# Kernel tuning notes

Measured on AMD Instinct MI355X. Metric: run time of the kernel, lower is better.

Reference implementation:

```python
import jax, jax.numpy as jnp
import numpy as np
import math

N_NODES = 50000
N_EDGES = 800000
DIM = 128
NUM_HEADS = 8
CUTOFF = 5.0


def setup_inputs() -> dict:
    key = jax.random.key(0)
    ks = jax.random.split(key, 12)
    s = 1.0 / math.sqrt(DIM)
    inp = {
        "x": jax.random.normal(ks[0], (N_NODES, DIM), dtype=jnp.float32),
        "edge_index": jax.random.randint(ks[1], (2, N_EDGES), 0, N_NODES, dtype=jnp.int32),
        "edge_attr": jax.random.normal(ks[2], (N_EDGES, DIM), dtype=jnp.float32),
        "edge_len": jax.random.uniform(ks[3], (N_EDGES,), dtype=jnp.float32) * CUTOFF,
        "W_Q": jax.random.normal(ks[4], (DIM, DIM), dtype=jnp.float32) * s,
        "b_Q": jnp.zeros((DIM,), dtype=jnp.float32),
        "W_K": jax.random.normal(ks[5], (DIM, DIM), dtype=jnp.float32) * s,
        "b_K": jnp.zeros((DIM,), dtype=jnp.float32),
        "W_V": jax.random.normal(ks[6], (DIM, DIM), dtype=jnp.float32) * s,
        "b_V": jnp.zeros((DIM,), dtype=jnp.float32),
        "W_O": jax.random.normal(ks[7], (DIM, DIM), dtype=jnp.float32) * s,
        "b_O": jnp.zeros((DIM,), dtype=jnp.float32),
    }
    return inp


def reference(x, edge_index, edge_attr, edge_len, W_Q, b_Q, W_K, b_K, W_V, b_V, W_O, b_O):
    num_nodes = x.shape[0]
    d_k = DIM // NUM_HEADS
    j = edge_index[1]  # target node per edge, [E]

    # edge-wise QKV: Q projected on nodes then gathered per edge; K/V from edge_attr
    query = (x @ W_Q + b_Q)[j]              # [E, D]
    key = edge_attr @ W_K + b_K             # [E, D]
    value = edge_attr @ W_V + b_V           # [E, D]

    # smooth cosine cutoff envelope, [E]
    phi_cutoff = 0.5 * (jnp.cos(jnp.pi * edge_len / CUTOFF) + 1.0)

    query = query.reshape(-1, NUM_HEADS, d_k)
    key = key.reshape(-1, NUM_HEADS, d_k)
    value = value.reshape(-1, NUM_HEADS, d_k)

    scores = (query * key).sum(axis=-1) / math.sqrt(d_k)  # [E, H]

    # segment softmax over edges grouped by target node j
    seg_max = jax.ops.segment_max(scores, j, num_segments=num_nodes)  # [N, H]
    ex = jnp.exp(scores - seg_max[j])                                 # [E, H]
    seg_sum = jax.ops.segment_sum(ex, j, num_segments=num_nodes)      # [N, H]
    alpha = ex / seg_sum[j]                                           # [E, H]

    attn_out = (alpha[..., None] * value * phi_cutoff[:, None, None]).reshape(-1, DIM)  # [E, D]
    node_out = jax.ops.segment_sum(attn_out, j, num_segments=num_nodes)                # [N, D]
    return node_out @ W_O + b_O
```

## Files before the change

### kernel.cpp

```cpp
#include <hip/hip_runtime.h>
#include <math.h>

#define NN 50000
#define NE 800000
#define D  128
#define NH 8

typedef __attribute__((ext_vector_type(8))) short bf16x8;
typedef __attribute__((ext_vector_type(4))) float f32x4;

__device__ __forceinline__ unsigned short f2bf(float f) {
  unsigned x = __float_as_uint(f);
  unsigned r = ((x >> 16) & 1u) + 0x7FFFu;
  return (unsigned short)((x + r) >> 16);
}

__device__ __forceinline__ void load_tile(const float* __restrict__ A, int row0, int M,
                                          float (*As)[65], int tid) {
#pragma unroll
  for (int i = 0; i < 8; ++i) {
    int p = tid + i * 256;
    int r = p >> 5;
    int c = (p & 31) << 2;
    float4 v = make_float4(0.f, 0.f, 0.f, 0.f);
    int row = row0 + r;
    if (row < M) v = *(const float4*)(A + (size_t)row * D + c);
    As[c + 0][r] = v.x;
    As[c + 1][r] = v.y;
    As[c + 2][r] = v.z;
    As[c + 3][r] = v.w;
  }
}

__device__ __forceinline__ void gemm_core(const float (*As)[65], const float* __restrict__ B,
                                          int ty, int tx, float acc[4][8]) {
#pragma unroll 8
  for (int k = 0; k < 128; ++k) {
    float a[4];
#pragma unroll
    for (int r = 0; r < 4; ++r) a[r] = As[k][ty * 4 + r];
    float4 b0 = *(const float4*)(B + k * D + tx * 8);
    float4 b1 = *(const float4*)(B + k * D + tx * 8 + 4);
    float b[8] = {b0.x, b0.y, b0.z, b0.w, b1.x, b1.y, b1.z, b1.w};
#pragma unroll
    for (int r = 0; r < 4; ++r)
#pragma unroll
      for (int c = 0; c < 8; ++c) acc[r][c] += a[r] * b[c];
  }
}

__global__ __launch_bounds__(256, 4) void gemm_bias_k(const float* __restrict__ A,
    const float* __restrict__ B, const float* __restrict__ bias,
    float* __restrict__ C, int M) {
  __shared__ float As[128][65];
  int tid = threadIdx.x;
  int row0 = blockIdx.x * 64;
  load_tile(A, row0, M, As, tid);
  __syncthreads();
  int ty = tid >> 4, tx = tid & 15;
  float acc[4][8] = {};
  gemm_core(As, B, ty, tx, acc);
  float4 ba = *(const float4*)(bias + tx * 8);
  float4 bb = *(const float4*)(bias + tx * 8 + 4);
#pragma unroll
  for (int r = 0; r < 4; ++r) {
    int row = row0 + ty * 4 + r;
    if (row < M) {
      float4 o0 = make_float4(acc[r][0] + ba.x, acc[r][1] + ba.y,
                              acc[r][2] + ba.z, acc[r][3] + ba.w);
      float4 o1 = make_float4(acc[r][4] + bb.x, acc[r][5] + bb.y,
                              acc[r][6] + bb.z, acc[r][7] + bb.w);
      *(float4*)(C + (size_t)row * D + tx * 8) = o0;
      *(float4*)(C + (size_t)row * D + tx * 8 + 4) = o1;
    }
  }
}

__global__ __launch_bounds__(256) void hist_k(const int* __restrict__ jidx,
                                              int* __restrict__ cnt) {
  int e = blockIdx.x * 256 + threadIdx.x;
  atomicAdd(&cnt[jidx[e]], 1);
}

__global__ __launch_bounds__(1024) void scan_k(const int* __restrict__ cnt,
    int* __restrict__ offs, int* __restrict__ cursor) {
  __shared__ int part[1024];
  const int CH = 49;
  int t = threadIdx.x;
  int base = t * CH;
  int s = 0;
  for (int i = 0; i < CH; ++i) {
    int idx = base + i;
    if (idx < NN) s += cnt[idx];
  }
  part[t] = s;
  __syncthreads();
  for (int off = 1; off < 1024; off <<= 1) {
    int v = (t >= off) ? part[t - off] : 0;
    __syncthreads();
    part[t] += v;
    __syncthreads();
  }
  int run = (t == 0) ? 0 : part[t - 1];
  for (int i = 0; i < CH; ++i) {
    int idx = base + i;
    if (idx < NN) {
      offs[idx] = run;
      cursor[idx] = run;
      run += cnt[idx];
    }
  }
  if (t == 1023) offs[NN] = run;
}

__global__ __launch_bounds__(256) void scatter_k(const int* __restrict__ jidx,
    int* __restrict__ cursor, int* __restrict__ pos) {
  int e = blockIdx.x * 256 + threadIdx.x;
  pos[e] = atomicAdd(&cursor[jidx[e]], 1);
}

__global__ __launch_bounds__(128) void wprep_k(const float* __restrict__ WK,
    const float* __restrict__ WV, unsigned short* __restrict__ WKVT) {
  int n = blockIdx.x;
  int k = threadIdx.x;
  const float* src = (n < 128) ? WK : WV;
  WKVT[n * 128 + k] = f2bf(src[(size_t)k * 128 + (n & 127)]);
}

__global__ __launch_bounds__(512, 8) void kv_mfma_k(
    const float* __restrict__ EA, const unsigned short* __restrict__ WKVT,
    const float* __restrict__ bK, const float* __restrict__ bV,
    const float* __restrict__ Q, const int* __restrict__ jidx,
    const float* __restrict__ elen, const int* __restrict__ pos,
    float* __restrict__ scores_csr, unsigned short* __restrict__ Vc) {
  __shared__ unsigned short As[64 * 128];
  __shared__ float St[64][8];
  __shared__ float Sphi[64];
  __shared__ int Spos[64];
  __shared__ int Sjn[64];
  int tid = threadIdx.x;
  int e0 = blockIdx.x * 64;

  if (tid < 64) {
    Spos[tid] = pos[e0 + tid];
    Sjn[tid] = jidx[e0 + tid];
    float ln = elen[e0 + tid];
    Sphi[tid] = 0.5f * (__cosf(ln * 0.628318530717958647f) + 1.0f);
  }
#pragma unroll
  for (int i = 0; i < 2; ++i) {
    int p = tid + i * 512;
    int r = p >> 4;
    int c = p & 15;
    const float* src = EA + (size_t)(e0 + r) * D + c * 8;
    float4 v0 = *(const float4*)src;
    float4 v1 = *(const float4*)(src + 4);
    unsigned q0 = f2bf(v0.x) | ((unsigned)f2bf(v0.y) << 16);
    unsigned q1 = f2bf(v0.z) | ((unsigned)f2bf(v0.w) << 16);
    unsigned q2 = f2bf(v1.x) | ((unsigned)f2bf(v1.y) << 16);
    unsigned q3 = f2bf(v1.z) | ((unsigned)f2bf(v1.w) << 16);
    *(uint4*)(As + r * 128 + ((c * 8) ^ ((r & 7) << 3))) = make_uint4(q0, q1, q2, q3);
  }

  int w = tid >> 6, l = tid & 63;
  int lr = l & 15, lg = l >> 4;
  const unsigned short* wb = WKVT + (size_t)(w * 32 + lr) * 128 + lg * 8;
  bf16x8 Bcur0 = *(const bf16x8*)(wb);
  bf16x8 Bcur1 = *(const bf16x8*)(wb + 16 * 128);
  f32x4 acc[4][2] = {};
  __syncthreads();

#pragma unroll
  for (int ks = 0; ks < 4; ++ks) {
    bf16x8 Bn0, Bn1;
    if (ks < 3) {
      Bn0 = *(const bf16x8*)(wb + (ks + 1) * 32);
      Bn1 = *(const bf16x8*)(wb + 16 * 128 + (ks + 1) * 32);
    }
#pragma unroll
    for (int mi = 0; mi < 4; ++mi) {
      int row = mi * 16 + lr;
      int ku = ks * 32 + lg * 8;
      bf16x8 a = *(const bf16x8*)(As + row * 128 + (ku ^ ((row & 7) << 3)));
      acc[mi][0] = __builtin_amdgcn_mfma_f32_16x16x32_bf16(a, Bcur0, acc[mi][0], 0, 0, 0);
      acc[mi][1] = __builtin_amdgcn_mfma_f32_16x16x32_bf16(a, Bcur1, acc[mi][1], 0, 0, 0);
    }
    if (ks < 3) { Bcur0 = Bn0; Bcur1 = Bn1; }
  }
  __syncthreads();

  if (w < 4) {
    float bk0 = bK[w * 32 + lr], bk1 = bK[w * 32 + 16 + lr];
#pragma unroll
    for (int mi = 0; mi < 4; ++mi)
#pragma unroll
      for (int r = 0; r < 4; ++r) {
        int erow = mi * 16 + lg * 4 + r;
        int jn = Sjn[erow];
        const float* qrow = Q + (size_t)jn * D + w * 32;
        float q0 = qrow[lr], q1 = qrow[16 + lr];
        float t0 = (acc[mi][0][r] + bk0) * q0;
        float t1 = (acc[mi][1][r] + bk1) * q1;
        t0 += __shfl_xor(t0, 1); t1 += __shfl_xor(t1, 1);
        t0 += __shfl_xor(t0, 2); t1 += __shfl_xor(t1, 2);
        t0 += __shfl_xor(t0, 4); t1 += __shfl_xor(t1, 4);
        t0 += __shfl_xor(t0, 8); t1 += __shfl_xor(t1, 8);
        if (lr == 0) {
          St[erow][w * 2] = t0 * 0.25f;
          St[erow][w * 2 + 1] = t1 * 0.25f;
        }
      }
  } else {
    float bv0 = bV[(w - 4) * 32 + lr], bv1 = bV[(w - 4) * 32 + 16 + lr];
    int c0 = (w - 4) * 32 + lr;
#pragma unroll
    for (int mi = 0; mi < 4; ++mi)
#pragma unroll
      for (int r = 0; r < 4; ++r) {
        int row = mi * 16 + lg * 4 + r;
        float ph = Sphi[row];
        int sw = (row & 7) << 3;
        As[row * 128 + (c0 ^ sw)] = f2bf((acc[mi][0][r] + bv0) * ph);
        As[row * 128 + ((c0 + 16) ^ sw)] = f2bf((acc[mi][1][r] + bv1) * ph);
      }
  }
  __syncthreads();

  if (tid < 128) {
    int row = tid >> 1, half = tid & 1;
    float4 s = *(const float4*)(&St[row][half * 4]);
    *(float4*)(scores_csr + (size_t)Spos[row] * NH + half * 4) = s;
  }
#pragma unroll
  for (int i = 0; i < 2; ++i) {
    int p = tid + i * 512;
    int row = p >> 4, c = p & 15;
    uint4 v = *(const uint4*)(As + row * 128 + ((c * 8) ^ ((row & 7) << 3)));
    *(uint4*)(Vc + (size_t)Spos[row] * D + c * 8) = v;
  }
}

__global__ __launch_bounds__(256) void finish_k(const unsigned short* __restrict__ Vc,
    const float* __restrict__ scores_csr, const int* __restrict__ offs,
    float* __restrict__ accum) {
  int tid = threadIdx.x;
  int n = blockIdx.x * 4 + (tid >> 6);
  int l = tid & 63;
  int hg = l >> 3;
  int o0 = offs[n], o1 = offs[n + 1];
  float m = -INFINITY, den = 0.f, a0 = 0.f, a1 = 0.f;
  const unsigned* base = (const unsigned*)Vc;
  for (int s = o0; s < o1; ++s) {
    float sc = scores_csr[(size_t)s * NH + hg];
    unsigned u = base[(size_t)s * 64 + l];
    float nm = fmaxf(m, sc);
    float c = __expf(m - nm);
    float wg = __expf(sc - nm);
    den = den * c + wg;
    a0 = a0 * c + wg * __uint_as_float(u << 16);
    a1 = a1 * c + wg * __uint_as_float(u & 0xFFFF0000u);
    m = nm;
  }
  float inv = (den > 0.f) ? 1.0f / den : 0.f;
  *(float2*)(accum + (size_t)n * D + l * 2) = make_float2(a0 * inv, a1 * inv);
}

extern "C" void kernel_launch(void* const* d_in, const int* in_sizes, int n_in,
                              void* d_out, int out_size, void* d_ws, size_t ws_size,
                              hipStream_t stream) {
  const float* x     = (const float*)d_in[0];
  const int*   eidx  = (const int*)d_in[1];
  const int*   jidx  = eidx + NE;
  const float* eattr = (const float*)d_in[2];
  const float* elen  = (const float*)d_in[3];
  const float* W_Q   = (const float*)d_in[4];
  const float* b_Q   = (const float*)d_in[5];
  const float* W_K   = (const float*)d_in[6];
  const float* b_K   = (const float*)d_in[7];
  const float* W_V   = (const float*)d_in[8];
  const float* b_V   = (const float*)d_in[9];
  const float* W_O   = (const float*)d_in[10];
  const float* b_O   = (const float*)d_in[11];
  float* out = (float*)d_out;

  char* ws = (char*)d_ws;
  float* Q          = (float*)ws;            ws += (size_t)NN * D * 4;
  float* scores_csr = (float*)ws;            ws += (size_t)NE * NH * 4;
  float* accum      = (float*)ws;            ws += (size_t)NN * D * 4;
  int*   cnt        = (int*)ws;              ws += (size_t)NN * 4;
  int*   offs       = (int*)ws;              ws += (size_t)(NN + 1) * 4;
  int*   cursor     = (int*)ws;              ws += (size_t)NN * 4;
  int*   pos        = (int*)ws;              ws += (size_t)NE * 4;
  unsigned short* Vc = (unsigned short*)ws;
  unsigned short* WKVT = (unsigned short*)cursor;

  hipMemsetAsync(cnt, 0, (size_t)NN * 4, stream);

  hist_k<<<NE / 256, 256, 0, stream>>>(jidx, cnt);
  scan_k<<<1, 1024, 0, stream>>>(cnt, offs, cursor);
  scatter_k<<<NE / 256, 256, 0, stream>>>(jidx, cursor, pos);
  wprep_k<<<256, 128, 0, stream>>>(W_K, W_V, WKVT);

  gemm_bias_k<<<(NN + 63) / 64, 256, 0, stream>>>(x, W_Q, b_Q, Q, NN);
  kv_mfma_k<<<NE / 64, 512, 0, stream>>>(eattr, WKVT, b_K, b_V, Q, jidx, elen,
                                         pos, scores_csr, Vc);
  finish_k<<<NN / 4, 256, 0, stream>>>(Vc, scores_csr, offs, accum);
  gemm_bias_k<<<(NN + 63) / 64, 256, 0, stream>>>(accum, W_O, b_O, out, NN);
}
```

Baseline: 1.173 ms.

## Fuse segment softmax aggregation into KV kernel using sorted edge runs and atomics

The K/V projection kernel now visits edges in target-sorted order through an edge list, gathering edge_attr rows indirectly. Within each 64-edge block it finds runs of edges that share a target node and reduces exp(score)-weighted values and exp sums over each run. The partial sums go to per-node numerator and denominator buffers with atomics, and the final output GEMM divides by the denominator while loading its tile. This removes the per-edge V and score staging buffers and the separate finish kernel. In exchange it drops the max subtraction from the softmax, which risks overflow for large scores, and it adds atomic traffic plus scattered reads of edge rows.

```diff
diff --git a/kernel.cpp b/kernel.cpp
--- a/kernel.cpp
+++ b/kernel.cpp
@@ -13,23 +13,6 @@
   unsigned x = __float_as_uint(f);
   unsigned r = ((x >> 16) & 1u) + 0x7FFFu;
   return (unsigned short)((x + r) >> 16);
-}
-
-__device__ __forceinline__ void load_tile(const float* __restrict__ A, int row0, int M,
-                                          float (*As)[65], int tid) {
-#pragma unroll
-  for (int i = 0; i < 8; ++i) {
-    int p = tid + i * 256;
-    int r = p >> 5;
-    int c = (p & 31) << 2;
-    float4 v = make_float4(0.f, 0.f, 0.f, 0.f);
-    int row = row0 + r;
-    if (row < M) v = *(const float4*)(A + (size_t)row * D + c);
-    As[c + 0][r] = v.x;
-    As[c + 1][r] = v.y;
-    As[c + 2][r] = v.z;
-    As[c + 3][r] = v.w;
-  }
 }
 
 __device__ __forceinline__ void gemm_core(const float (*As)[65], const float* __restrict__ B,
@@ -49,17 +32,9 @@
   }
 }
 
-__global__ __launch_bounds__(256, 4) void gemm_bias_k(const float* __restrict__ A,
-    const float* __restrict__ B, const float* __restrict__ bias,
-    float* __restrict__ C, int M) {
-  __shared__ float As[128][65];
-  int tid = threadIdx.x;
-  int row0 = blockIdx.x * 64;
-  load_tile(A, row0, M, As, tid);
-  __syncthreads();
-  int ty = tid >> 4, tx = tid & 15;
-  float acc[4][8] = {};
-  gemm_core(As, B, ty, tx, acc);
+__device__ __forceinline__ void gemm_epilogue(float acc[4][8], const float* __restrict__ bias,
+                                              float* __restrict__ C, int row0, int ty, int tx,
+                                              int M) {
   float4 ba = *(const float4*)(bias + tx * 8);
   float4 bb = *(const float4*)(bias + tx * 8 + 4);
 #pragma unroll
@@ -74,6 +49,57 @@
       *(float4*)(C + (size_t)row * D + tx * 8 + 4) = o1;
     }
   }
+}
+
+__global__ __launch_bounds__(256, 4) void gemm_bias_k(const float* __restrict__ A,
+    const float* __restrict__ B, const float* __restrict__ bias,
+    float* __restrict__ C, int M) {
+  __shared__ float As[128][65];
+  int tid = threadIdx.x;
+  int row0 = blockIdx.x * 64;
+#pragma unroll
+  for (int i = 0; i < 8; ++i) {
+    int p = tid + i * 256;
+    int r = p >> 5;
+    int c = (p & 31) << 2;
+    float4 v = make_float4(0.f, 0.f, 0.f, 0.f);
+    int row = row0 + r;
+    if (row < M) v = *(const float4*)(A + (size_t)row * D + c);
+    As[c + 0][r] = v.x; As[c + 1][r] = v.y; As[c + 2][r] = v.z; As[c + 3][r] = v.w;
+  }
+  __syncthreads();
+  int ty = tid >> 4, tx = tid & 15;
+  float acc[4][8] = {};
+  gemm_core(As, B, ty, tx, acc);
+  gemm_epilogue(acc, bias, C, row0, ty, tx, M);
+}
+
+__global__ __launch_bounds__(256, 4) void gemm_norm_bias_k(const float* __restrict__ A,
+    const float* __restrict__ den, const float* __restrict__ B,
+    const float* __restrict__ bias, float* __restrict__ C, int M) {
+  __shared__ float As[128][65];
+  int tid = threadIdx.x;
+  int row0 = blockIdx.x * 64;
+#pragma unroll
+  for (int i = 0; i < 8; ++i) {
+    int p = tid + i * 256;
+    int r = p >> 5;
+    int c = (p & 31) << 2;
+    float4 v = make_float4(0.f, 0.f, 0.f, 0.f);
+    int row = row0 + r;
+    if (row < M) {
+      v = *(const float4*)(A + (size_t)row * D + c);
+      float dd = den[(size_t)row * NH + (c >> 4)];
+      float inv = (dd > 0.f) ? 1.0f / dd : 0.f;
+      v.x *= inv; v.y *= inv; v.z *= inv; v.w *= inv;
+    }
+    As[c + 0][r] = v.x; As[c + 1][r] = v.y; As[c + 2][r] = v.z; As[c + 3][r] = v.w;
+  }
+  __syncthreads();
+  int ty = tid >> 4, tx = tid & 15;
+  float acc[4][8] = {};
+  gemm_core(As, B, ty, tx, acc);
+  gemm_epilogue(acc, bias, C, row0, ty, tx, M);
 }
 
 __global__ __launch_bounds__(256) void hist_k(const int* __restrict__ jidx,
@@ -114,9 +140,10 @@
 }
 
 __global__ __launch_bounds__(256) void scatter_k(const int* __restrict__ jidx,
-    int* __restrict__ cursor, int* __restrict__ pos) {
+    int* __restrict__ cursor, int* __restrict__ elist) {
   int e = blockIdx.x * 256 + threadIdx.x;
-  pos[e] = atomicAdd(&cursor[jidx[e]], 1);
+  int p = atomicAdd(&cursor[jidx[e]], 1);
+  elist[p] = e;
 }
 
 __global__ __launch_bounds__(128) void wprep_k(const float* __restrict__ WK,
@@ -127,32 +154,40 @@
   WKVT[n * 128 + k] = f2bf(src[(size_t)k * 128 + (n & 127)]);
 }
 
-__global__ __launch_bounds__(512, 8) void kv_mfma_k(
+__global__ __launch_bounds__(512, 8) void kvagg_k(
     const float* __restrict__ EA, const unsigned short* __restrict__ WKVT,
     const float* __restrict__ bK, const float* __restrict__ bV,
     const float* __restrict__ Q, const int* __restrict__ jidx,
-    const float* __restrict__ elen, const int* __restrict__ pos,
-    float* __restrict__ scores_csr, unsigned short* __restrict__ Vc) {
-  __shared__ unsigned short As[64 * 128];
-  __shared__ float St[64][8];
+    const float* __restrict__ elen, const int* __restrict__ elist,
+    float* __restrict__ Pnum, float* __restrict__ Pden) {
+  __shared__ __align__(16) float VtF[64][132];
+  __shared__ float Sex[64][8];
   __shared__ float Sphi[64];
-  __shared__ int Spos[64];
   __shared__ int Sjn[64];
+  __shared__ int Sed[64];
+  __shared__ int runStart[65];
+  __shared__ int runNode[64];
+  __shared__ int nrunsS;
+  unsigned short* As = (unsigned short*)&VtF[0][0];
+
   int tid = threadIdx.x;
   int e0 = blockIdx.x * 64;
 
   if (tid < 64) {
-    Spos[tid] = pos[e0 + tid];
-    Sjn[tid] = jidx[e0 + tid];
-    float ln = elen[e0 + tid];
+    int eo = elist[e0 + tid];
+    Sed[tid] = eo;
+    Sjn[tid] = jidx[eo];
+    float ln = elen[eo];
     Sphi[tid] = 0.5f * (__cosf(ln * 0.628318530717958647f) + 1.0f);
   }
+  __syncthreads();
+
 #pragma unroll
   for (int i = 0; i < 2; ++i) {
     int p = tid + i * 512;
     int r = p >> 4;
     int c = p & 15;
-    const float* src = EA + (size_t)(e0 + r) * D + c * 8;
+    const float* src = EA + (size_t)Sed[r] * D + c * 8;
     float4 v0 = *(const float4*)src;
     float4 v1 = *(const float4*)(src + 4);
     unsigned q0 = f2bf(v0.x) | ((unsigned)f2bf(v0.y) << 16);
@@ -188,6 +223,21 @@
     if (ks < 3) { Bcur0 = Bn0; Bcur1 = Bn1; }
   }
   __syncthreads();
+
+  if (tid < 64) {
+    int flag = (tid == 0) || (Sjn[tid] != Sjn[tid - 1]);
+    unsigned long long mask = __ballot(flag);
+    int nr = __popcll(mask);
+    if (flag) {
+      int ri = __popcll(mask & ((1ull << tid) - 1ull));
+      runStart[ri] = tid;
+      runNode[ri] = Sjn[tid];
+    }
+    if (tid == 0) {
+      nrunsS = nr;
+      runStart[nr] = 64;
+    }
+  }
 
   if (w < 4) {
     float bk0 = bK[w * 32 + lr], bk1 = bK[w * 32 + 16 + lr];
@@ -206,8 +256,8 @@
         t0 += __shfl_xor(t0, 4); t1 += __shfl_xor(t1, 4);
         t0 += __shfl_xor(t0, 8); t1 += __shfl_xor(t1, 8);
         if (lr == 0) {
-          St[erow][w * 2] = t0 * 0.25f;
-          St[erow][w * 2 + 1] = t1 * 0.25f;
+          Sex[erow][w * 2] = __expf(t0 * 0.25f);
+          Sex[erow][w * 2 + 1] = __expf(t1 * 0.25f);
         }
       }
   } else {
@@ -219,50 +269,28 @@
       for (int r = 0; r < 4; ++r) {
         int row = mi * 16 + lg * 4 + r;
         float ph = Sphi[row];
-        int sw = (row & 7) << 3;
-        As[row * 128 + (c0 ^ sw)] = f2bf((acc[mi][0][r] + bv0) * ph);
-        As[row * 128 + ((c0 + 16) ^ sw)] = f2bf((acc[mi][1][r] + bv1) * ph);
+        VtF[row][c0] = (acc[mi][0][r] + bv0) * ph;
+        VtF[row][c0 + 16] = (acc[mi][1][r] + bv1) * ph;
       }
   }
   __syncthreads();
 
-  if (tid < 128) {
-    int row = tid >> 1, half = tid & 1;
-    float4 s = *(const float4*)(&St[row][half * 4]);
-    *(float4*)(scores_csr + (size_t)Spos[row] * NH + half * 4) = s;
-  }
-#pragma unroll
-  for (int i = 0; i < 2; ++i) {
-    int p = tid + i * 512;
-    int row = p >> 4, c = p & 15;
-    uint4 v = *(const uint4*)(As + row * 128 + ((c * 8) ^ ((row & 7) << 3)));
-    *(uint4*)(Vc + (size_t)Spos[row] * D + c * 8) = v;
-  }
-}
-
-__global__ __launch_bounds__(256) void finish_k(const unsigned short* __restrict__ Vc,
-    const float* __restrict__ scores_csr, const int* __restrict__ offs,
-    float* __restrict__ accum) {
-  int tid = threadIdx.x;
-  int n = blockIdx.x * 4 + (tid >> 6);
-  int l = tid & 63;
-  int hg = l >> 3;
-  int o0 = offs[n], o1 = offs[n + 1];
-  float m = -INFINITY, den = 0.f, a0 = 0.f, a1 = 0.f;
-  const unsigned* base = (const unsigned*)Vc;
-  for (int s = o0; s < o1; ++s) {
-    float sc = scores_csr[(size_t)s * NH + hg];
-    unsigned u = base[(size_t)s * 64 + l];
-    float nm = fmaxf(m, sc);
-    float c = __expf(m - nm);
-    float wg = __expf(sc - nm);
-    den = den * c + wg;
-    a0 = a0 * c + wg * __uint_as_float(u << 16);
-    a1 = a1 * c + wg * __uint_as_float(u & 0xFFFF0000u);
-    m = nm;
-  }
-  float inv = (den > 0.f) ? 1.0f / den : 0.f;
-  *(float2*)(accum + (size_t)n * D + l * 2) = make_float2(a0 * inv, a1 * inv);
+  int nr = nrunsS;
+  int col = tid & 127;
+  int h = col >> 4;
+  for (int ri = tid >> 7; ri < nr; ri += 4) {
+    int r0 = runStart[ri], r1 = runStart[ri + 1];
+    float s = 0.f;
+    for (int r = r0; r < r1; ++r) s += VtF[r][col] * Sex[r][h];
+    atomicAdd(&Pnum[(size_t)runNode[ri] * D + col], s);
+  }
+  if (tid < nr * NH) {
+    int ri = tid >> 3, hh = tid & 7;
+    int r0 = runStart[ri], r1 = runStart[ri + 1];
+    float s = 0.f;
+    for (int r = r0; r < r1; ++r) s += Sex[r][hh];
+    atomicAdd(&Pden[(size_t)runNode[ri] * NH + hh], s);
+  }
 }
 
 extern "C" void kernel_launch(void* const* d_in, const int* in_sizes, int n_in,
@@ -284,26 +312,25 @@
   float* out = (float*)d_out;
 
   char* ws = (char*)d_ws;
-  float* Q          = (float*)ws;            ws += (size_t)NN * D * 4;
-  float* scores_csr = (float*)ws;            ws += (size_t)NE * NH * 4;
-  float* accum      = (float*)ws;            ws += (size_t)NN * D * 4;
-  int*   cnt        = (int*)ws;              ws += (size_t)NN * 4;
-  int*   offs       = (int*)ws;              ws += (size_t)(NN + 1) * 4;
-  int*   cursor     = (int*)ws;              ws += (size_t)NN * 4;
-  int*   pos        = (int*)ws;              ws += (size_t)NE * 4;
-  unsigned short* Vc = (unsigned short*)ws;
+  float* Q     = (float*)ws;             ws += (size_t)NN * D * 4;
+  float* Pnum  = (float*)ws;             ws += (size_t)NN * D * 4;
+  float* Pden  = (float*)ws;             ws += (size_t)NN * NH * 4;
+  int*   cnt   = (int*)ws;               ws += (size_t)NN * 4;
+  int*   offs  = (int*)ws;               ws += (size_t)(NN + 1) * 4;
+  int*   cursor= (int*)ws;               ws += (size_t)NN * 4;
+  int*   elist = (int*)ws;               ws += (size_t)NE * 4;
   unsigned short* WKVT = (unsigned short*)cursor;
 
   hipMemsetAsync(cnt, 0, (size_t)NN * 4, stream);
+  hipMemsetAsync(Pnum, 0, (size_t)NN * (D + NH) * 4, stream);
 
   hist_k<<<NE / 256, 256, 0, stream>>>(jidx, cnt);
   scan_k<<<1, 1024, 0, stream>>>(cnt, offs, cursor);
-  scatter_k<<<NE / 256, 256, 0, stream>>>(jidx, cursor, pos);
+  scatter_k<<<NE / 256, 256, 0, stream>>>(jidx, cursor, elist);
   wprep_k<<<256, 128, 0, stream>>>(W_K, W_V, WKVT);
 
   gemm_bias_k<<<(NN + 63) / 64, 256, 0, stream>>>(x, W_Q, b_Q, Q, NN);
-  kv_mfma_k<<<NE / 64, 512, 0, stream>>>(eattr, WKVT, b_K, b_V, Q, jidx, elen,
-                                         pos, scores_csr, Vc);
-  finish_k<<<NN / 4, 256, 0, stream>>>(Vc, scores_csr, offs, accum);
-  gemm_bias_k<<<(NN + 63) / 64, 256, 0, stream>>>(accum, W_O, b_O, out, NN);
-}
+  kvagg_k<<<NE / 64, 512, 0, stream>>>(eattr, WKVT, b_K, b_V, Q, jidx, elen,
+                                       elist, Pnum, Pden);
+  gemm_norm_bias_k<<<(NN + 63) / 64, 256, 0, stream>>>(Pnum, Pden, W_O, b_O, out, NN);
+}
```

Measured after the change: 1.042 ms. -11.1%, faster.
